# Kernel tuning notes

Measured on AMD Instinct MI355X. Metric: run time of the kernel, lower is better.

Reference implementation:

```python
import jax, jax.numpy as jnp
import numpy as np

B, C, H, W = 8, 21, 512, 512  # n_classes=21 (VOC-style semantic segmentation)


def setup_inputs() -> dict:
    key = jax.random.key(0)
    k1, k2, k3 = jax.random.split(key, 3)
    # Dirichlet-ish positive inputs (unnormalized); forward normalizes rows.
    prior = jax.random.uniform(k1, (B, C, H, W), dtype=jnp.float32) + 1e-3
    current = jax.random.uniform(k2, (B, C, H, W), dtype=jnp.float32) + 1e-3
    cm = jax.random.uniform(k3, (C, C), dtype=jnp.float32) + 1e-3
    confusion_matrix = cm / cm.sum(axis=1, keepdims=True)  # rows are states (distributions)
    return {"prior": prior, "current": current, "confusion_matrix": confusion_matrix}


def reference(prior, current, confusion_matrix):
    n_classes = confusion_matrix.shape[0]
    # [B, C, H, W] -> [B*H*W, C]
    p = jnp.transpose(prior, (0, 2, 3, 1)).reshape(-1, n_classes)
    c = jnp.transpose(current, (0, 2, 3, 1)).reshape(-1, n_classes)
    # Row-normalize to multinomial distributions
    p = p / p.sum(axis=1, keepdims=True)
    c = c / c.sum(axis=1, keepdims=True)
    # Bayes fusion: pred(i) = sum_j CM[i, j] * current[j]  ->  c @ CM^T
    pred = c @ confusion_matrix.T            # [N, C]
    post = p * pred                          # elementwise likelihood update
    post = post / post.sum(axis=1, keepdims=True)
    return post                              # [B*H*W, C]
```

## Files before the change

### kernel.cpp

```cpp
#include <hip/hip_runtime.h>
#include <stdint.h>

#define CC   21
#define HWp  262144
#define NPIX 2097152
#define PAD  257

__global__ __launch_bounds__(256, 6)
void ep_kernel(const float* __restrict__ prior,
               const float* __restrict__ current,
               const float* __restrict__ cm,
               float* __restrict__ out)
{
    __shared__ float cmT[CC * CC];
    __shared__ float stage[CC * PAD];

    const int tid = threadIdx.x;
    for (int k = tid; k < CC * CC; k += 256) {
        int j = k / CC, i = k - j * CC;
        cmT[k] = cm[i * CC + j];
    }
    __syncthreads();

    const int n0   = blockIdx.x * 256 + tid;
    const int b    = n0 >> 18;
    const int hw   = n0 & (HWp - 1);
    const int base = b * (CC << 18) + hw;

    float q[CC];
#pragma unroll
    for (int i = 0; i < CC; i++) q[i] = 0.f;

#pragma unroll
    for (int j = 0; j < CC; j++) {
        float c = current[base + j * HWp];
        const float* w = &cmT[j * CC];
#pragma unroll
        for (int i = 0; i < CC; i++) q[i] = fmaf(w[i], c, q[i]);
    }

    float s = 0.f;
#pragma unroll
    for (int i = 0; i < CC; i++) {
        float p = prior[base + i * HWp];
        q[i] *= p;
        s += q[i];
    }
    const float r = 1.f / s;

#pragma unroll
    for (int i = 0; i < CC; i++) stage[i * PAD + tid] = q[i] * r;
    __syncthreads();

    const int bb = blockIdx.x * (256 * CC);
#pragma unroll
    for (int it = 0; it < CC; it++) {
        int m = it * 256 + tid;
        int t = m / CC;
        int i = m - t * CC;
        out[bb + m] = stage[i * PAD + t];
    }
}

extern "C" void kernel_launch(void* const* d_in, const int* in_sizes, int n_in,
                              void* d_out, int out_size, void* d_ws, size_t ws_size,
                              hipStream_t stream) {
    const float* prior   = (const float*)d_in[0];
    const float* current = (const float*)d_in[1];
    const float* cm      = (const float*)d_in[2];
    float* out           = (float*)d_out;

    dim3 grid(NPIX / 256), block(256);
    ep_kernel<<<grid, block, 0, stream>>>(prior, current, cm, out);
}
```

Measured before the change: 393.5 us.

## Process two pixels per thread with float2 loads and software-pipelined batches

Each thread now handles two adjacent pixels using float2 loads, so every LDS read of a confusion-matrix weight feeds two FMAs and fewer global load instructions are issued. Loads of current and prior are split into batches of seven and interleaved with the compute to overlap memory latency. The confusion matrix rows are padded to 24 floats, the transpose staging runs in two halves with extra barriers, and launch bounds drop to 5 waves. Register pressure roughly doubles, which may reduce occupancy.

```diff
diff --git a/kernel.cpp b/kernel.cpp
--- a/kernel.cpp
+++ b/kernel.cpp
@@ -4,61 +4,107 @@
 #define CC   21
 #define HWp  262144
 #define NPIX 2097152
-#define PAD  257
+#define CMS  24
+#define PAD  258
+#define PXB  512
+#define NT   256
 
-__global__ __launch_bounds__(256, 6)
+
+template<int J0>
+__device__ __forceinline__ void load7(const float* __restrict__ src, int base, float2* buf) {
+#pragma unroll
+    for (int u = 0; u < 7; u++)
+        buf[u] = *(const float2*)(src + base + (J0 + u) * HWp);
+}
+
+template<int J0>
+__device__ __forceinline__ void fma7(const float* cmT, const float2* buf, float2* q) {
+#pragma unroll
+    for (int u = 0; u < 7; u++) {
+        const float* wrow = &cmT[(J0 + u) * CMS];
+        const float cx = buf[u].x, cy = buf[u].y;
+#pragma unroll
+        for (int i = 0; i < CC; i++) {
+            q[i].x = fmaf(wrow[i], cx, q[i].x);
+            q[i].y = fmaf(wrow[i], cy, q[i].y);
+        }
+    }
+}
+
+template<int I0>
+__device__ __forceinline__ void mul7(const float2* buf, float2* q, float& sx, float& sy) {
+#pragma unroll
+    for (int u = 0; u < 7; u++) {
+        q[I0 + u].x *= buf[u].x; sx += q[I0 + u].x;
+        q[I0 + u].y *= buf[u].y; sy += q[I0 + u].y;
+    }
+}
+
+__global__ __launch_bounds__(256, 5)
 void ep_kernel(const float* __restrict__ prior,
                const float* __restrict__ current,
                const float* __restrict__ cm,
                float* __restrict__ out)
 {
-    __shared__ float cmT[CC * CC];
-    __shared__ float stage[CC * PAD];
+    __shared__ __align__(16) float cmT[CC * CMS];
+    __shared__ __align__(16) float stage[CC * PAD];
 
     const int tid = threadIdx.x;
-    for (int k = tid; k < CC * CC; k += 256) {
-        int j = k / CC, i = k - j * CC;
-        cmT[k] = cm[i * CC + j];
+    for (int k = tid; k < CC * CMS; k += NT) {
+        int j = k / CMS, i = k - j * CMS;
+        cmT[k] = (i < CC) ? cm[i * CC + j] : 0.f;
     }
     __syncthreads();
 
-    const int n0   = blockIdx.x * 256 + tid;
+    const int n0   = blockIdx.x * PXB + tid * 2;
     const int b    = n0 >> 18;
     const int hw   = n0 & (HWp - 1);
     const int base = b * (CC << 18) + hw;
 
-    float q[CC];
+    float2 q[CC];
 #pragma unroll
-    for (int i = 0; i < CC; i++) q[i] = 0.f;
+    for (int i = 0; i < CC; i++) { q[i].x = 0.f; q[i].y = 0.f; }
 
+    float2 A[7], Bb[7];
+    load7<0>(current, base, A);
+    load7<7>(current, base, Bb);
+    fma7<0>(cmT, A, q);
+    load7<14>(current, base, A);
+    fma7<7>(cmT, Bb, q);
+    load7<0>(prior, base, Bb);
+    fma7<14>(cmT, A, q);
+
+    float sx = 0.f, sy = 0.f;
+    load7<7>(prior, base, A);
+    mul7<0>(Bb, q, sx, sy);
+    load7<14>(prior, base, Bb);
+    mul7<7>(A, q, sx, sy);
+    mul7<14>(Bb, q, sx, sy);
+
+    const float rx = 1.f / sx, ry = 1.f / sy;
+
+    const int bb = blockIdx.x * (PXB * CC);
 #pragma unroll
-    for (int j = 0; j < CC; j++) {
-        float c = current[base + j * HWp];
-        const float* w = &cmT[j * CC];
+    for (int h = 0; h < 2; h++) {
+        if ((tid >> 7) == h) {
+            const int px = (tid & 127) * 2;
+            float2* srow;
 #pragma unroll
-        for (int i = 0; i < CC; i++) q[i] = fmaf(w[i], c, q[i]);
-    }
-
-    float s = 0.f;
+            for (int i = 0; i < CC; i++) {
+                srow = (float2*)&stage[i * PAD + px];
+                float2 v; v.x = q[i].x * rx; v.y = q[i].y * ry;
+                *srow = v;
+            }
+        }
+        __syncthreads();
 #pragma unroll
-    for (int i = 0; i < CC; i++) {
-        float p = prior[base + i * HWp];
-        q[i] *= p;
-        s += q[i];
-    }
-    const float r = 1.f / s;
-
-#pragma unroll
-    for (int i = 0; i < CC; i++) stage[i * PAD + tid] = q[i] * r;
-    __syncthreads();
-
-    const int bb = blockIdx.x * (256 * CC);
-#pragma unroll
-    for (int it = 0; it < CC; it++) {
-        int m = it * 256 + tid;
-        int t = m / CC;
-        int i = m - t * CC;
-        out[bb + m] = stage[i * PAD + t];
+        for (int it = 0; it < CC; it++) {
+            int m = it * NT + tid;
+            int t = m / CC;
+            int i = m - t * CC;
+            out[bb + h * (NT * CC) + m] = stage[i * PAD + t];
+        }
+        __syncthreads();
     }
 }
 
@@ -70,6 +116,6 @@
     const float* cm      = (const float*)d_in[2];
     float* out           = (float*)d_out;
 
-    dim3 grid(NPIX / 256), block(256);
+    dim3 grid(NPIX / PXB), block(NT);
     ep_kernel<<<grid, block, 0, stream>>>(prior, current, cm, out);
 }
```

Result: slower. 402.5 us (+2.3%).

## Stage prior and current loads into LDS via async global_load_lds

Applied to the files above, without the earlier changes.

Each wave now issues asynchronous global-to-LDS copies for all 42 channel values of its pixels before the confusion-matrix staging, then reads the inputs from shared memory. The aim is to put every input load in flight early and overlap it with the cmT setup. The cmT rows are also padded to 24 floats. The shared buffer is reused as the output staging area, which needs an extra barrier, and launch bounds drop to 3 blocks per CU because the kernel now uses more LDS.

```diff
diff --git a/kernel.cpp b/kernel.cpp
--- a/kernel.cpp
+++ b/kernel.cpp
@@ -1,31 +1,56 @@
 #include <hip/hip_runtime.h>
 #include <stdint.h>
 
-#define CC   21
-#define HWp  262144
-#define NPIX 2097152
-#define PAD  257
+#define CC    21
+#define HWp   262144
+#define NPIX  2097152
+#define CMS   24
+#define PAD   257
+#define NT    256
 
-__global__ __launch_bounds__(256, 6)
+
+__device__ __forceinline__ void async_copy4(float* lds_dst, const float* g_src) {
+    __builtin_amdgcn_global_load_lds(
+        (__attribute__((address_space(1))) void*)(g_src),
+        (__attribute__((address_space(3))) void*)(lds_dst),
+        4, 0, 0);
+}
+
+__global__ __launch_bounds__(256, 3)
 void ep_kernel(const float* __restrict__ prior,
                const float* __restrict__ current,
                const float* __restrict__ cm,
                float* __restrict__ out)
 {
-    __shared__ float cmT[CC * CC];
-    __shared__ float stage[CC * PAD];
+    __shared__ __align__(16) char smem[4 * 42 * 64 * sizeof(float)];
+    __shared__ __align__(16) float cmT[CC * CMS];
 
-    const int tid = threadIdx.x;
-    for (int k = tid; k < CC * CC; k += 256) {
-        int j = k / CC, i = k - j * CC;
-        cmT[k] = cm[i * CC + j];
-    }
-    __syncthreads();
+    float* const ib    = (float*)smem;
+    float* const stage = (float*)smem;
 
-    const int n0   = blockIdx.x * 256 + tid;
+    const int tid  = threadIdx.x;
+    const int w    = tid >> 6;
+    const int lane = tid & 63;
+
+    const int n0   = blockIdx.x * NT + tid;
     const int b    = n0 >> 18;
     const int hw   = n0 & (HWp - 1);
     const int base = b * (CC << 18) + hw;
+
+    float* const wbuf = ib + (w * 42) * 64;
+    (void)lane;
+#pragma unroll
+    for (int j = 0; j < CC; j++)
+        async_copy4(wbuf + j * 64, current + base + j * HWp);
+#pragma unroll
+    for (int i = 0; i < CC; i++)
+        async_copy4(wbuf + (CC + i) * 64, prior + base + i * HWp);
+
+    for (int k = tid; k < CC * CMS; k += NT) {
+        int j = k / CMS, i = k - j * CMS;
+        cmT[k] = (i < CC) ? cm[i * CC + j] : 0.f;
+    }
+    __syncthreads();
 
     float q[CC];
 #pragma unroll
@@ -33,29 +58,30 @@
 
 #pragma unroll
     for (int j = 0; j < CC; j++) {
-        float c = current[base + j * HWp];
-        const float* w = &cmT[j * CC];
+        const float c = wbuf[j * 64 + lane];
+        const float* wrow = &cmT[j * CMS];
 #pragma unroll
-        for (int i = 0; i < CC; i++) q[i] = fmaf(w[i], c, q[i]);
+        for (int i = 0; i < CC; i++) q[i] = fmaf(wrow[i], c, q[i]);
     }
 
     float s = 0.f;
 #pragma unroll
     for (int i = 0; i < CC; i++) {
-        float p = prior[base + i * HWp];
+        const float p = wbuf[(CC + i) * 64 + lane];
         q[i] *= p;
         s += q[i];
     }
     const float r = 1.f / s;
 
+    __syncthreads();
 #pragma unroll
     for (int i = 0; i < CC; i++) stage[i * PAD + tid] = q[i] * r;
     __syncthreads();
 
-    const int bb = blockIdx.x * (256 * CC);
+    const int bb = blockIdx.x * (NT * CC);
 #pragma unroll
     for (int it = 0; it < CC; it++) {
-        int m = it * 256 + tid;
+        int m = it * NT + tid;
         int t = m / CC;
         int i = m - t * CC;
         out[bb + m] = stage[i * PAD + t];
@@ -70,6 +96,6 @@
     const float* cm      = (const float*)d_in[2];
     float* out           = (float*)d_out;
 
-    dim3 grid(NPIX / 256), block(256);
+    dim3 grid(NPIX / NT), block(NT);
     ep_kernel<<<grid, block, 0, stream>>>(prior, current, cm, out);
 }
```

New measurement: 401.4 us. 2.0% more time.
